# Performance work log

Measured on AMD Instinct MI355X. Metric: run time of the kernel, lower is better.

## Reference

```python
import jax, jax.numpy as jnp
import numpy as np

N_NODES = 50000
N_EDGES = 800000
IN_CH = 128
HIDDEN = 256
OUT_DIM = 1
N_GRAPHS = 64


def setup_inputs() -> dict:
    key = jax.random.key(0)
    ks = jax.random.split(key, 9)
    x = jax.random.normal(ks[0], (N_NODES, IN_CH), dtype=jnp.float32)
    edge_index = jax.random.randint(ks[1], (2, N_EDGES), 0, N_NODES)
    batch = jnp.sort(jax.random.randint(ks[2], (N_NODES,), 0, N_GRAPHS))
    # GCNConv weight (lin has no bias; bias added after aggregation in PyG)
    w1 = jax.random.normal(ks[3], (IN_CH, HIDDEN), dtype=jnp.float32) * 0.05
    b1 = jnp.zeros((HIDDEN,), dtype=jnp.float32)
    # FFNN head
    w2 = jax.random.normal(ks[4], (HIDDEN, HIDDEN), dtype=jnp.float32) * 0.05
    b2 = jnp.zeros((HIDDEN,), dtype=jnp.float32)
    w3 = jax.random.normal(ks[5], (HIDDEN, OUT_DIM), dtype=jnp.float32) * 0.05
    b3 = jnp.zeros((OUT_DIM,), dtype=jnp.float32)
    return {"x": x, "edge_index": edge_index, "batch": batch,
            "w1": w1, "b1": b1, "w2": w2, "b2": b2, "w3": w3, "b3": b3}


def reference(x, edge_index, batch, w1, b1, w2, b2, w3, b3):
    N = x.shape[0]
    # --- GCNConv: symmetric-normalized aggregation with self-loops ---
    loop = jnp.arange(N)
    src = jnp.concatenate([edge_index[0], loop])  # [E+N]
    dst = jnp.concatenate([edge_index[1], loop])  # [E+N]
    h = x @ w1  # transform first (in_ch -> hidden), PyG order
    deg = jax.ops.segment_sum(jnp.ones_like(dst, dtype=h.dtype), dst, num_segments=N)
    deg_inv_sqrt = jnp.where(deg > 0, jax.lax.rsqrt(deg), 0.0)
    norm = deg_inv_sqrt[src] * deg_inv_sqrt[dst]  # [E+N]
    msg = h[src] * norm[:, None]  # [E+N, hidden]
    h = jax.ops.segment_sum(msg, dst, num_segments=N) + b1  # [N, hidden]
    h = jax.nn.relu(h)
    # --- global_mean_pool over batch ids ---
    cnt = jax.ops.segment_sum(jnp.ones((N,), dtype=h.dtype), batch, num_segments=N_GRAPHS)
    pooled = jax.ops.segment_sum(h, batch, num_segments=N_GRAPHS)
    pooled = pooled / jnp.maximum(cnt, 1.0)[:, None]  # [G, hidden]
    # --- FFNN head (dropout is identity in eval mode) ---
    z = jax.nn.relu(pooled @ w2 + b2)
    return z @ w3 + b3  # [G, out_dim]
```

## Files before the change

kernel.cpp:

```cpp
#include <hip/hip_runtime.h>

#define IN_CH   128
#define HIDDEN  256
#define N_GRAPHS 64
#define GN 64
#define NPB 64
#define LOGNPB 6
#define MAXBUCK 1024
#define NBLK 400

typedef short short8 __attribute__((ext_vector_type(8)));
typedef float f32x4 __attribute__((ext_vector_type(4)));

__device__ inline unsigned f2bf(float f) {
  unsigned u = __float_as_uint(f);
  return (u + 0x7fffu + ((u >> 16) & 1u)) >> 16;
}
__device__ inline unsigned pack2(float lo, float hi) {
  return (f2bf(hi) << 16) | f2bf(lo);
}
__device__ inline void acc8(uint4 v, float w, float* A) {
  A[0] += w * __uint_as_float(v.x << 16);
  A[1] += w * __uint_as_float(v.x & 0xffff0000u);
  A[2] += w * __uint_as_float(v.y << 16);
  A[3] += w * __uint_as_float(v.y & 0xffff0000u);
  A[4] += w * __uint_as_float(v.z << 16);
  A[5] += w * __uint_as_float(v.z & 0xffff0000u);
  A[6] += w * __uint_as_float(v.w << 16);
  A[7] += w * __uint_as_float(v.w & 0xffff0000u);
}

__global__ __launch_bounds__(256) void k_p1(
    const float* __restrict__ x, ushort* __restrict__ xh,
    const float* __restrict__ w1, ushort* __restrict__ w1t,
    const int* __restrict__ dst, int* __restrict__ ghist,
    float* __restrict__ pooled, int total8, int e, int nbuck, int chunk) {
  __shared__ int h[MAXBUCK];
  int t = threadIdx.x, b = blockIdx.x;
  for (int k = t; k < nbuck; k += 256) h[k] = 0;
  int gid = b * 256 + t;
  const int nthr = NBLK * 256;
  for (int i = gid; i < total8; i += nthr) {
    const float4* xp = reinterpret_cast<const float4*>(x) + (size_t)i * 2;
    float4 a = xp[0], bb = xp[1];
    uint4 o;
    o.x = pack2(a.x, a.y);
    o.y = pack2(a.z, a.w);
    o.z = pack2(bb.x, bb.y);
    o.w = pack2(bb.z, bb.w);
    reinterpret_cast<uint4*>(xh)[i] = o;
  }
  if (gid < HIDDEN * IN_CH) {
    int nn = gid >> 7, k = gid & 127;
    w1t[gid] = (ushort)f2bf(w1[k * 256 + nn]);
  }
  if (gid < N_GRAPHS * HIDDEN) pooled[gid] = 0.f;
  __syncthreads();
  int s = b * chunk, eend = min(e, s + chunk);
  for (int i = s + t; i < eend; i += 256) atomicAdd(&h[dst[i] >> LOGNPB], 1);
  __syncthreads();
  for (int k = t; k < nbuck; k += 256) ghist[b * MAXBUCK + k] = h[k];
}

__global__ __launch_bounds__(512) void k_p2a(const int* __restrict__ ghist,
    int* __restrict__ boff, int* __restrict__ total, int nbuck) {
  __shared__ int sm[512];
  int k = blockIdx.x, t = threadIdx.x;
  int v = (t < NBLK) ? ghist[t * MAXBUCK + k] : 0;
  sm[t] = v;
  __syncthreads();
  for (int d = 1; d < 512; d <<= 1) {
    int add = (t >= d) ? sm[t - d] : 0;
    __syncthreads();
    sm[t] += add;
    __syncthreads();
  }
  if (t < NBLK) boff[k * NBLK + t] = sm[t] - v;
  if (t == 511) total[k] = sm[511];
}

__global__ __launch_bounds__(256) void k_p3(
    const int* __restrict__ src, const int* __restrict__ dst,
    const int* __restrict__ boff, const int* __restrict__ total,
    int* __restrict__ ebuf, int e, int nbuck, int chunk) {
  __shared__ int cur[MAXBUCK];
  __shared__ int ts[256];
  int t = threadIdx.x, b = blockIdx.x;
  int t4 = t * 4;
  int v0 = (t4 + 0 < nbuck) ? total[t4 + 0] : 0;
  int v1 = (t4 + 1 < nbuck) ? total[t4 + 1] : 0;
  int v2 = (t4 + 2 < nbuck) ? total[t4 + 2] : 0;
  int v3 = (t4 + 3 < nbuck) ? total[t4 + 3] : 0;
  int lsum = v0 + v1 + v2 + v3;
  ts[t] = lsum;
  __syncthreads();
  for (int d = 1; d < 256; d <<= 1) {
    int add = (t >= d) ? ts[t - d] : 0;
    __syncthreads();
    ts[t] += add;
    __syncthreads();
  }
  int base = ts[t] - lsum;
  cur[t4 + 0] = base;
  cur[t4 + 1] = base + v0;
  cur[t4 + 2] = base + v0 + v1;
  cur[t4 + 3] = base + v0 + v1 + v2;
  __syncthreads();
  for (int k = t; k < nbuck; k += 256) cur[k] += boff[k * NBLK + b];
  __syncthreads();
  int s = b * chunk, eend = min(e, s + chunk);
  for (int i = s + t; i < eend; i += 256) {
    int d = dst[i];
    int pos = atomicAdd(&cur[d >> LOGNPB], 1);
    ebuf[pos] = (src[i] & 0xffff) | ((d & (NPB - 1)) << 16);
  }
}

__global__ __launch_bounds__(256) void k_p4(const int* __restrict__ ebuf,
    const int* __restrict__ total, ushort* __restrict__ csr, int* __restrict__ offs,
    float* __restrict__ dinv, int n, int nbuck, int etot) {
  __shared__ int dcnt[NPB];
  __shared__ int doff[NPB];
  __shared__ int dcur[NPB];
  __shared__ int red[256];
  int k = blockIdx.x, t = threadIdx.x;
  int partial = 0;
  for (int i = t; i < k; i += 256) partial += total[i];
  red[t] = partial;
  if (t < NPB) dcnt[t] = 0;
  __syncthreads();
  for (int d = 128; d > 0; d >>= 1) {
    if (t < d) red[t] += red[t + d];
    __syncthreads();
  }
  int s = red[0];
  int eend = s + total[k];
  for (int i = s + t; i < eend; i += 256)
    atomicAdd(&dcnt[(ebuf[i] >> 16) & (NPB - 1)], 1);
  __syncthreads();
  if (t < NPB) doff[t] = dcnt[t];
  __syncthreads();
  for (int d = 1; d < NPB; d <<= 1) {
    int add = 0;
    if (t < NPB && t >= d) add = doff[t - d];
    __syncthreads();
    if (t < NPB) doff[t] += add;
    __syncthreads();
  }
  if (t < NPB) {
    int ex = doff[t] - dcnt[t];
    dcur[t] = s + ex;
    int node = k * NPB + t;
    if (node < n) {
      offs[node] = s + ex;
      dinv[node] = 1.0f / sqrtf((float)(dcnt[t] + 1));
    }
  }
  if (k == nbuck - 1 && t == 0) offs[n] = etot;
  __syncthreads();
  for (int i = s + t; i < eend; i += 256) {
    int v = ebuf[i];
    int pos = atomicAdd(&dcur[(v >> 16) & (NPB - 1)], 1);
    csr[pos] = (ushort)v;
  }
}

__global__ __launch_bounds__(256) void k_agg(const ushort* __restrict__ xh,
    const ushort* __restrict__ csr, const int* __restrict__ offs,
    const float* __restrict__ dinv, ushort* __restrict__ yh, int n) {
  int node = blockIdx.x * 4 + (threadIdx.x >> 6);
  if (node >= n) return;
  int lane = threadIdx.x & 63;
  int es = lane >> 4;
  int cg = lane & 15;
  int o = offs[node];
  int c = offs[node + 1] - o;
  float A[8] = {0.f, 0.f, 0.f, 0.f, 0.f, 0.f, 0.f, 0.f};
  for (int it = 0; it < c; it += 16) {
    float w[4];
    uint4 v[4];
#pragma unroll
    for (int u = 0; u < 4; ++u) {
      int ii = it + u * 4 + es;
      bool val = ii < c;
      int s = val ? (int)csr[o + ii] : 0;
      w[u] = val ? dinv[s] : 0.f;
      v[u] = *reinterpret_cast<const uint4*>(&xh[(size_t)s * IN_CH + cg * 8]);
    }
#pragma unroll
    for (int u = 0; u < 4; ++u) acc8(v[u], w[u], A);
  }
#pragma unroll
  for (int k = 0; k < 8; ++k) {
    A[k] += __shfl_xor(A[k], 16, 64);
    A[k] += __shfl_xor(A[k], 32, 64);
  }
  if (es == 0) {
    float dn = dinv[node];
    uint4 xs = *reinterpret_cast<const uint4*>(&xh[(size_t)node * IN_CH + cg * 8]);
    float xv[8] = {0.f, 0.f, 0.f, 0.f, 0.f, 0.f, 0.f, 0.f};
    acc8(xs, dn, xv);
    float v[8];
#pragma unroll
    for (int k = 0; k < 8; ++k) v[k] = (A[k] + xv[k]) * dn;
    uint4 w;
    w.x = pack2(v[0], v[1]);
    w.y = pack2(v[2], v[3]);
    w.z = pack2(v[4], v[5]);
    w.w = pack2(v[6], v[7]);
    *reinterpret_cast<uint4*>(&yh[(size_t)node * IN_CH + cg * 8]) = w;
  }
}

__global__ __launch_bounds__(256) void k_gemmpool(
    const ushort* __restrict__ yh, const ushort* __restrict__ w1t,
    const float* __restrict__ b1, const int* __restrict__ batch,
    float* __restrict__ pooled, int n) {
  __shared__ float part[4][HIDDEN];
  __shared__ int bl[GN];
  int t = threadIdx.x;
  int node0 = blockIdx.x * GN;

  if (t < GN) {
    int nd = node0 + t;
    bl[t] = (nd < n) ? batch[nd] : -1;
  }
  {
    float* pp = &part[0][0];
    for (int i = t; i < 4 * HIDDEN; i += 256) pp[i] = 0.f;
  }

  int wv = t >> 6, l = t & 63;
  int lr = l & 15;
  int lk = l >> 4;
  int colbase = wv * 64;

  f32x4 acc[4][4];
#pragma unroll
  for (int m = 0; m < 4; ++m)
#pragma unroll
    for (int nn = 0; nn < 4; ++nn) acc[m][nn] = (f32x4){0.f, 0.f, 0.f, 0.f};

#pragma unroll
  for (int kc = 0; kc < 4; ++kc) {
    short8 a[4], b[4];
#pragma unroll
    for (int m = 0; m < 4; ++m)
      a[m] = *reinterpret_cast<const short8*>(
          &yh[(size_t)(node0 + m * 16 + lr) * IN_CH + kc * 32 + lk * 8]);
#pragma unroll
    for (int nn = 0; nn < 4; ++nn)
      b[nn] = *reinterpret_cast<const short8*>(
          &w1t[(size_t)(colbase + nn * 16 + lr) * IN_CH + kc * 32 + lk * 8]);
#pragma unroll
    for (int m = 0; m < 4; ++m)
#pragma unroll
      for (int nn = 0; nn < 4; ++nn)
        acc[m][nn] = __builtin_amdgcn_mfma_f32_16x16x32_bf16(a[m], b[nn], acc[m][nn], 0, 0, 0);
  }

  __syncthreads();

  float bias[4];
#pragma unroll
  for (int nn = 0; nn < 4; ++nn) bias[nn] = b1[colbase + nn * 16 + lr];
  int g0 = bl[0];

#pragma unroll
  for (int m = 0; m < 4; ++m) {
    float s[4] = {0.f, 0.f, 0.f, 0.f};
    int gcur = -1;
#pragma unroll
    for (int j = 0; j < 4; ++j) {
      int row = m * 16 + lk * 4 + j;
      int node = node0 + row;
      int g = (node < n) ? bl[row] : -1;
      if (g != gcur) {
        if (gcur >= 0) {
          int gi = gcur - g0;
          if (gi < 4) {
#pragma unroll
            for (int nn = 0; nn < 4; ++nn)
              atomicAdd(&part[gi][colbase + nn * 16 + lr], s[nn]);
          } else {
#pragma unroll
            for (int nn = 0; nn < 4; ++nn)
              atomicAdd(&pooled[gcur * HIDDEN + colbase + nn * 16 + lr], s[nn]);
          }
        }
#pragma unroll
        for (int u = 0; u < 4; ++u) s[u] = 0.f;
        gcur = g;
      }
      if (g >= 0) {
#pragma unroll
        for (int nn = 0; nn < 4; ++nn)
          s[nn] += fmaxf(acc[m][nn][j] + bias[nn], 0.f);
      }
    }
    if (gcur >= 0) {
      int gi = gcur - g0;
      if (gi < 4) {
#pragma unroll
        for (int nn = 0; nn < 4; ++nn)
          atomicAdd(&part[gi][colbase + nn * 16 + lr], s[nn]);
      } else {
#pragma unroll
        for (int nn = 0; nn < 4; ++nn)
          atomicAdd(&pooled[gcur * HIDDEN + colbase + nn * 16 + lr], s[nn]);
      }
    }
  }

  __syncthreads();
  int lastIdx = min(GN, n - node0) - 1;
  int gmax = bl[lastIdx];
  int span = gmax - g0;
  if (span > 3) span = 3;
  for (int gi = 0; gi <= span; ++gi) {
    atomicAdd(&pooled[(g0 + gi) * HIDDEN + t], part[gi][t]);
  }
}

__global__ __launch_bounds__(256) void k_head(const float* __restrict__ pooled,
    const int* __restrict__ batch, int n, const float* __restrict__ w2,
    const float* __restrict__ b2, const float* __restrict__ w3,
    const float* __restrict__ b3, float* __restrict__ out) {
  __shared__ float p[256];
  __shared__ float red[4];
  __shared__ int scnt;
  int g = blockIdx.x, t = threadIdx.x;
  if (t == 0) {
    int lo = 0, hi = n;
    while (lo < hi) { int mid = (lo + hi) >> 1; if (batch[mid] < g) lo = mid + 1; else hi = mid; }
    int a = lo;
    lo = 0; hi = n;
    int g1 = g + 1;
    while (lo < hi) { int mid = (lo + hi) >> 1; if (batch[mid] < g1) lo = mid + 1; else hi = mid; }
    scnt = lo - a;
  }
  __syncthreads();
  float c = (float)max(scnt, 1);
  p[t] = pooled[g * HIDDEN + t] / c;
  __syncthreads();
  float a = 0.f;
  for (int k = 0; k < 256; ++k) a += p[k] * w2[k * 256 + t];
  a += b2[t];
  a = fmaxf(a, 0.f);
  float part = a * w3[t];
  for (int off = 32; off > 0; off >>= 1) part += __shfl_down(part, off, 64);
  if ((t & 63) == 0) red[t >> 6] = part;
  __syncthreads();
  if (t == 0) out[g] = red[0] + red[1] + red[2] + red[3] + b3[0];
}

extern "C" void kernel_launch(void* const* d_in, const int* in_sizes, int n_in,
                              void* d_out, int out_size, void* d_ws, size_t ws_size,
                              hipStream_t stream) {
  const float* x    = (const float*)d_in[0];
  const int*   ei   = (const int*)d_in[1];
  const int*   batch= (const int*)d_in[2];
  const float* w1   = (const float*)d_in[3];
  const float* b1   = (const float*)d_in[4];
  const float* w2   = (const float*)d_in[5];
  const float* b2   = (const float*)d_in[6];
  const float* w3   = (const float*)d_in[7];
  const float* b3   = (const float*)d_in[8];
  float* out = (float*)d_out;

  int N = in_sizes[2];
  int E = in_sizes[1] / 2;
  const int* esrc = ei;
  const int* edst = ei + E;
  int nbuck = (N + NPB - 1) / NPB;
  int chunk = (E + NBLK - 1) / NBLK;

  int* W = (int*)d_ws;
  int*    ebuf   = W;
  int*    base1  = W + (size_t)E;
  float*  pooled = (float*)base1;
  int*    offs   = base1 + N_GRAPHS * HIDDEN;
  float*  dinv   = (float*)(offs + N + 1);
  int*    total  = (int*)(dinv + N);
  int*    ghist  = total + MAXBUCK;
  int*    boff   = ghist + NBLK * MAXBUCK;
  ushort* csr    = (ushort*)(boff + MAXBUCK * NBLK);
  int*    after_csr = boff + MAXBUCK * NBLK + (E + 1) / 2;
  ushort* w1t    = (ushort*)after_csr;
  ushort* xh     = (ushort*)(after_csr + 16384);
  ushort* yh     = xh + (size_t)N * IN_CH;

  int total8 = N * 16;
  k_p1<<<NBLK, 256, 0, stream>>>(x, xh, w1, w1t, edst, ghist, pooled,
                                 total8, E, nbuck, chunk);
  k_p2a<<<nbuck, 512, 0, stream>>>(ghist, boff, total, nbuck);
  k_p3<<<NBLK, 256, 0, stream>>>(esrc, edst, boff, total, ebuf, E, nbuck, chunk);
  k_p4<<<nbuck, 256, 0, stream>>>(ebuf, total, csr, offs, dinv, N, nbuck, E);
  k_agg<<<(N + 3) / 4, 256, 0, stream>>>(xh, csr, offs, dinv, yh, N);
  k_gemmpool<<<(N + GN - 1) / GN, 256, 0, stream>>>(yh, w1t, b1, batch, pooled, N);
  k_head<<<N_GRAPHS, 256, 0, stream>>>(pooled, batch, N, w2, b2, w3, b3, out);
}
```

Measured before the change: 123.9 us.

## Fuse aggregation into GEMM-pool kernel via LDS staging; transpose histogram layout

The neighbour-aggregation kernel is merged into the GEMM+pool kernel. Each block aggregates its 64 nodes (16 per wave) into a padded LDS tile, then feeds that tile straight to the MFMA GEMM. This removes the round trip of the intermediate yh array through global memory and one kernel launch. The cost is fewer blocks (782 instead of 12500) and per-wave serial node loops, which may give less latency hiding on the gathers. The histogram is also stored bucket-major so the scan kernel reads it contiguously.

```diff
diff --git a/kernel.cpp b/kernel.cpp
--- a/kernel.cpp
+++ b/kernel.cpp
@@ -4,6 +4,7 @@
 #define HIDDEN  256
 #define N_GRAPHS 64
 #define GN 64
+#define YLS 136
 #define NPB 64
 #define LOGNPB 6
 #define MAXBUCK 1024
@@ -59,14 +60,14 @@
   int s = b * chunk, eend = min(e, s + chunk);
   for (int i = s + t; i < eend; i += 256) atomicAdd(&h[dst[i] >> LOGNPB], 1);
   __syncthreads();
-  for (int k = t; k < nbuck; k += 256) ghist[b * MAXBUCK + k] = h[k];
+  for (int k = t; k < nbuck; k += 256) ghist[k * NBLK + b] = h[k];
 }
 
 __global__ __launch_bounds__(512) void k_p2a(const int* __restrict__ ghist,
     int* __restrict__ boff, int* __restrict__ total, int nbuck) {
   __shared__ int sm[512];
   int k = blockIdx.x, t = threadIdx.x;
-  int v = (t < NBLK) ? ghist[t * MAXBUCK + k] : 0;
+  int v = (t < NBLK) ? ghist[k * NBLK + t] : 0;
   sm[t] = v;
   __syncthreads();
   for (int d = 1; d < 512; d <<= 1) {
@@ -165,57 +166,12 @@
   }
 }
 
-__global__ __launch_bounds__(256) void k_agg(const ushort* __restrict__ xh,
-    const ushort* __restrict__ csr, const int* __restrict__ offs,
-    const float* __restrict__ dinv, ushort* __restrict__ yh, int n) {
-  int node = blockIdx.x * 4 + (threadIdx.x >> 6);
-  if (node >= n) return;
-  int lane = threadIdx.x & 63;
-  int es = lane >> 4;
-  int cg = lane & 15;
-  int o = offs[node];
-  int c = offs[node + 1] - o;
-  float A[8] = {0.f, 0.f, 0.f, 0.f, 0.f, 0.f, 0.f, 0.f};
-  for (int it = 0; it < c; it += 16) {
-    float w[4];
-    uint4 v[4];
-#pragma unroll
-    for (int u = 0; u < 4; ++u) {
-      int ii = it + u * 4 + es;
-      bool val = ii < c;
-      int s = val ? (int)csr[o + ii] : 0;
-      w[u] = val ? dinv[s] : 0.f;
-      v[u] = *reinterpret_cast<const uint4*>(&xh[(size_t)s * IN_CH + cg * 8]);
-    }
-#pragma unroll
-    for (int u = 0; u < 4; ++u) acc8(v[u], w[u], A);
-  }
-#pragma unroll
-  for (int k = 0; k < 8; ++k) {
-    A[k] += __shfl_xor(A[k], 16, 64);
-    A[k] += __shfl_xor(A[k], 32, 64);
-  }
-  if (es == 0) {
-    float dn = dinv[node];
-    uint4 xs = *reinterpret_cast<const uint4*>(&xh[(size_t)node * IN_CH + cg * 8]);
-    float xv[8] = {0.f, 0.f, 0.f, 0.f, 0.f, 0.f, 0.f, 0.f};
-    acc8(xs, dn, xv);
-    float v[8];
-#pragma unroll
-    for (int k = 0; k < 8; ++k) v[k] = (A[k] + xv[k]) * dn;
-    uint4 w;
-    w.x = pack2(v[0], v[1]);
-    w.y = pack2(v[2], v[3]);
-    w.z = pack2(v[4], v[5]);
-    w.w = pack2(v[6], v[7]);
-    *reinterpret_cast<uint4*>(&yh[(size_t)node * IN_CH + cg * 8]) = w;
-  }
-}
-
-__global__ __launch_bounds__(256) void k_gemmpool(
-    const ushort* __restrict__ yh, const ushort* __restrict__ w1t,
-    const float* __restrict__ b1, const int* __restrict__ batch,
-    float* __restrict__ pooled, int n) {
+__global__ __launch_bounds__(256) void k_aggemm(
+    const ushort* __restrict__ xh, const ushort* __restrict__ csr,
+    const int* __restrict__ offs, const float* __restrict__ dinv,
+    const ushort* __restrict__ w1t, const float* __restrict__ b1,
+    const int* __restrict__ batch, float* __restrict__ pooled, int n) {
+  __shared__ ushort ylds[GN * YLS];
   __shared__ float part[4][HIDDEN];
   __shared__ int bl[GN];
   int t = threadIdx.x;
@@ -230,6 +186,54 @@
     for (int i = t; i < 4 * HIDDEN; i += 256) pp[i] = 0.f;
   }
 
+  {
+    int wv = t >> 6, lane = t & 63;
+    int es = lane >> 4, cg = lane & 15;
+    for (int r = 0; r < 16; ++r) {
+      int row = wv * 16 + r;
+      int node = node0 + row;
+      if (node >= n) break;
+      int o = offs[node];
+      int c = offs[node + 1] - o;
+      float A[8] = {0.f, 0.f, 0.f, 0.f, 0.f, 0.f, 0.f, 0.f};
+      for (int it = 0; it < c; it += 16) {
+        float w[4];
+        uint4 v[4];
+#pragma unroll
+        for (int u = 0; u < 4; ++u) {
+          int ii = it + u * 4 + es;
+          bool val = ii < c;
+          int s = val ? (int)csr[o + ii] : 0;
+          w[u] = val ? dinv[s] : 0.f;
+          v[u] = *reinterpret_cast<const uint4*>(&xh[(size_t)s * IN_CH + cg * 8]);
+        }
+#pragma unroll
+        for (int u = 0; u < 4; ++u) acc8(v[u], w[u], A);
+      }
+#pragma unroll
+      for (int k = 0; k < 8; ++k) {
+        A[k] += __shfl_xor(A[k], 16, 64);
+        A[k] += __shfl_xor(A[k], 32, 64);
+      }
+      if (es == 0) {
+        float dn = dinv[node];
+        uint4 xs = *reinterpret_cast<const uint4*>(&xh[(size_t)node * IN_CH + cg * 8]);
+        float xv[8] = {0.f, 0.f, 0.f, 0.f, 0.f, 0.f, 0.f, 0.f};
+        acc8(xs, dn, xv);
+        float vv[8];
+#pragma unroll
+        for (int k = 0; k < 8; ++k) vv[k] = (A[k] + xv[k]) * dn;
+        uint4 w;
+        w.x = pack2(vv[0], vv[1]);
+        w.y = pack2(vv[2], vv[3]);
+        w.z = pack2(vv[4], vv[5]);
+        w.w = pack2(vv[6], vv[7]);
+        *reinterpret_cast<uint4*>(&ylds[row * YLS + cg * 8]) = w;
+      }
+    }
+  }
+  __syncthreads();
+
   int wv = t >> 6, l = t & 63;
   int lr = l & 15;
   int lk = l >> 4;
@@ -247,7 +251,7 @@
 #pragma unroll
     for (int m = 0; m < 4; ++m)
       a[m] = *reinterpret_cast<const short8*>(
-          &yh[(size_t)(node0 + m * 16 + lr) * IN_CH + kc * 32 + lk * 8]);
+          &ylds[(m * 16 + lr) * YLS + kc * 32 + lk * 8]);
 #pragma unroll
     for (int nn = 0; nn < 4; ++nn)
       b[nn] = *reinterpret_cast<const short8*>(
@@ -258,8 +262,6 @@
       for (int nn = 0; nn < 4; ++nn)
         acc[m][nn] = __builtin_amdgcn_mfma_f32_16x16x32_bf16(a[m], b[nn], acc[m][nn], 0, 0, 0);
   }
-
-  __syncthreads();
 
   float bias[4];
 #pragma unroll
@@ -388,7 +390,6 @@
   int*    after_csr = boff + MAXBUCK * NBLK + (E + 1) / 2;
   ushort* w1t    = (ushort*)after_csr;
   ushort* xh     = (ushort*)(after_csr + 16384);
-  ushort* yh     = xh + (size_t)N * IN_CH;
 
   int total8 = N * 16;
   k_p1<<<NBLK, 256, 0, stream>>>(x, xh, w1, w1t, edst, ghist, pooled,
@@ -396,7 +397,7 @@
   k_p2a<<<nbuck, 512, 0, stream>>>(ghist, boff, total, nbuck);
   k_p3<<<NBLK, 256, 0, stream>>>(esrc, edst, boff, total, ebuf, E, nbuck, chunk);
   k_p4<<<nbuck, 256, 0, stream>>>(ebuf, total, csr, offs, dinv, N, nbuck, E);
-  k_agg<<<(N + 3) / 4, 256, 0, stream>>>(xh, csr, offs, dinv, yh, N);
-  k_gemmpool<<<(N + GN - 1) / GN, 256, 0, stream>>>(yh, w1t, b1, batch, pooled, N);
+  k_aggemm<<<(N + GN - 1) / GN, 256, 0, stream>>>(xh, csr, offs, dinv,
+                                                  w1t, b1, batch, pooled, N);
   k_head<<<N_GRAPHS, 256, 0, stream>>>(pooled, batch, N, w2, b2, w3, b3, out);
 }
```

Measured after the change: 173.4 us. 1.4x slower.
